# Kernel optimization log

Measured on AMD Instinct MI355X. Metric: run time of the kernel, lower is better.

## Reference

```python
import jax, jax.numpy as jnp
import numpy as np

B_, L_, D_MODEL, D_STATE, D_CONV, EXPAND, N_BLOCKS = 2, 2048, 512, 16, 4, 2, 4
D_INNER = EXPAND * D_MODEL            # 1024
DT_RANK = (D_MODEL + 15) // 16        # 32 (ceil(d_model/16))


def setup_inputs() -> dict:
    key = jax.random.key(0)
    ks = jax.random.split(key, 8)
    s = 0.02
    n = N_BLOCKS
    x = jax.random.normal(ks[0], (B_, L_, D_MODEL), jnp.float32)
    W_in = jax.random.normal(ks[1], (n, D_MODEL, 2 * D_INNER), jnp.float32) * s
    conv_w = jax.random.normal(ks[2], (n, D_INNER, D_CONV), jnp.float32) * s
    conv_b = jnp.zeros((n, D_INNER), jnp.float32)
    W_x = jax.random.normal(ks[3], (n, D_INNER, DT_RANK + 2 * D_STATE), jnp.float32) * s
    W_dt = jax.random.normal(ks[4], (n, DT_RANK, D_INNER), jnp.float32) * s
    # dt bias so softplus(b_dt) gives small positive timesteps (standard Mamba init range)
    b_dt = jax.random.uniform(ks[5], (n, D_INNER), jnp.float32, minval=-4.6, maxval=-2.3)
    # A_log init: log(1..d_state) per channel (S4D-real init)
    A_log = jnp.log(jnp.broadcast_to(jnp.arange(1, D_STATE + 1, dtype=jnp.float32), (n, D_INNER, D_STATE)))
    Dp = jnp.ones((n, D_INNER), jnp.float32)
    W_out = jax.random.normal(ks[6], (n, D_INNER, D_MODEL), jnp.float32) * s
    return {"x": x, "W_in": W_in, "conv_w": conv_w, "conv_b": conv_b,
            "W_x": W_x, "W_dt": W_dt, "b_dt": b_dt, "A_log": A_log,
            "Dp": Dp, "W_out": W_out}


def _scan_combine(e1, e2):
    a1, b1 = e1
    a2, b2 = e2
    return a1 * a2, a2 * b1 + b2


def _mamba_block(x, W_in, conv_w, conv_b, W_x, W_dt, b_dt, A_log, Dp, W_out):
    # x: [B, L, d_model]
    xz = x @ W_in                                   # [B, L, 2*d_inner]
    xi, z = jnp.split(xz, 2, axis=-1)
    # causal depthwise conv over time (torch pads d_conv-1 then truncates to L)
    xc = jnp.transpose(xi, (0, 2, 1))               # [B, d_inner, L]
    w = conv_w[:, None, :]                          # [d_inner, 1, d_conv]
    xc = jax.lax.conv_general_dilated(
        xc, w, window_strides=(1,), padding=[(D_CONV - 1, 0)],
        dimension_numbers=("NCH", "OIH", "NCH"), feature_group_count=D_INNER)
    xc = xc + conv_b[None, :, None]
    xc = jax.nn.silu(jnp.transpose(xc, (0, 2, 1)))  # [B, L, d_inner]
    # input-dependent dt, B, C
    dbc = xc @ W_x                                  # [B, L, dt_rank + 2*d_state]
    dt_raw = dbc[..., :DT_RANK]
    Bs = dbc[..., DT_RANK:DT_RANK + D_STATE]        # [B, L, d_state]
    Cs = dbc[..., DT_RANK + D_STATE:]               # [B, L, d_state]
    dt = jax.nn.softplus(dt_raw @ W_dt + b_dt)      # [B, L, d_inner]
    A = -jnp.exp(A_log)                             # [d_inner, d_state]
    # discretized selective scan terms
    dA = jnp.exp(dt[..., None] * A)                 # [B, L, d_inner, d_state]
    dBx = (dt * xc)[..., None] * Bs[:, :, None, :]  # [B, L, d_inner, d_state]
    # parallel associative scan over time: h_t = dA_t * h_{t-1} + dBx_t
    _, h = jax.lax.associative_scan(_scan_combine, (dA, dBx), axis=1)
    y = jnp.einsum("blds,bls->bld", h, Cs) + xc * Dp
    y = y * jax.nn.silu(z)
    return y @ W_out                                # [B, L, d_model]


def reference(x, W_in, conv_w, conv_b, W_x, W_dt, b_dt, A_log, Dp, W_out):
    for i in range(N_BLOCKS):
        resid = x
        x = _mamba_block(x, W_in[i], conv_w[i], conv_b[i], W_x[i], W_dt[i],
                         b_dt[i], A_log[i], Dp[i], W_out[i])
        x = x + resid
    return x
```

## Files before the change

### kernel.cpp

```cpp
#include <hip/hip_runtime.h>


#define L_    2048
#define DM    512
#define DI    1024
#define DS    16
#define NBLK  4
#define NC    64
#define CH    32
#define MROWS 4096

using u16 = unsigned short;
typedef __bf16 bf16x8 __attribute__((ext_vector_type(8)));
typedef float  f32x4  __attribute__((ext_vector_type(4)));

__device__ __forceinline__ float b2f(u16 u) {
    union { unsigned int i; float f; } v; v.i = ((unsigned int)u) << 16; return v.f;
}
__device__ __forceinline__ u16 f2b(float f) {
    union { float f; unsigned int i; } v; v.f = f;
    unsigned int x = v.i;
    return (u16)((x + 0x7FFFu + ((x >> 16) & 1u)) >> 16);
}
__device__ __forceinline__ float silu_(float x) { return x / (1.f + __expf(-x)); }

struct F4 { float x, y, z, w; };
__device__ __forceinline__ F4 load4(const void* p, size_t e, bool isbf) {
    F4 r;
    if (isbf) {
        ushort4 v = *(const ushort4*)((const u16*)p + e);
        r.x = b2f(v.x); r.y = b2f(v.y); r.z = b2f(v.z); r.w = b2f(v.w);
    } else {
        float4 v = *(const float4*)((const float*)p + e);
        r.x = v.x; r.y = v.y; r.z = v.z; r.w = v.w;
    }
    return r;
}
__device__ __forceinline__ float load1(const void* p, size_t e, bool isbf) {
    return isbf ? b2f(((const u16*)p)[e]) : ((const float*)p)[e];
}

__device__ __forceinline__ void async16(const u16* g, u16* l) {
    __builtin_amdgcn_global_load_lds(
        (const __attribute__((address_space(1))) unsigned int*)g,
        (__attribute__((address_space(3))) unsigned int*)l, 16, 0, 0);
}

__global__ void probe_dtype(const void* x, float* flag) {
    __shared__ int allok;
    if (threadIdx.x == 0) allok = 1;
    __syncthreads();
    const u16* p = (const u16*)x;
    bool ok = true;
    for (int i = threadIdx.x; i < 2048; i += 256) {
        float v = b2f(p[i]);
        if (!(v == v) || fabsf(v) >= 1000.f) ok = false;
    }
    if (!ok) allok = 0;
    __syncthreads();
    if (threadIdx.x == 0) flag[0] = allok ? 1.f : 0.f;
}

__global__ __launch_bounds__(256) void transpose_wb(
    const void* __restrict__ src, int R, int C,
    u16* __restrict__ dst, const float* __restrict__ flagp)
{
    const bool isbf = (*flagp > 0.5f);
    __shared__ u16 t[32][33];
    const size_t mo = (size_t)blockIdx.z * R * C;
    const int c0 = blockIdx.x * 32, r0 = blockIdx.y * 32;
    const int tx = threadIdx.x & 31, ty = threadIdx.x >> 5;
    #pragma unroll
    for (int i = 0; i < 32; i += 8)
        t[ty + i][tx] = f2b(load1(src, mo + (size_t)(r0 + ty + i) * C + c0 + tx, isbf));
    __syncthreads();
    #pragma unroll
    for (int i = 0; i < 32; i += 8)
        dst[mo + (size_t)(c0 + ty + i) * R + r0 + tx] = t[tx][ty + i];
}

template<int BN, int MT, int OM>
__global__ __launch_bounds__(256) void gemm_lds(
    const u16* __restrict__ A, int lda,
    const u16* __restrict__ BT, int Kd,
    u16* __restrict__ Cb, float* __restrict__ Cf, int ldc,
    const float* __restrict__ resid)
{
    constexpr int BM = 32 * MT;
    constexpr int NT = BN / 32;
    constexpr int W  = NT * 16;
    constexpr int CA = BM * 4;
    constexpr int T  = CA + BN * 4;
    constexpr int PW = T / 4;
    constexpr int NI = PW / 64;
    constexpr int STG = (BM + BN) * 32;
    constexpr int EPI = 4 * 16 * (W + 4) * 2;
    constexpr int LN  = STG > EPI ? STG : EPI;
    __shared__ u16 sL[LN];
    u16* sA = sL;
    u16* sB = sL + BM * 32;
    const int tid = threadIdx.x;
    const int lane = tid & 63;
    const int wid = tid >> 6;
    const int wm = wid >> 1, wn = wid & 1;
    const int m0 = blockIdx.y * BM;
    const int n0 = blockIdx.x * BN;
    const int col16 = lane & 15, quad = lane >> 4;

    f32x4 acc[MT][NT];
    #pragma unroll
    for (int i = 0; i < MT; i++)
        #pragma unroll
        for (int j = 0; j < NT; j++) acc[i][j] = {0.f, 0.f, 0.f, 0.f};

    for (int k0 = 0; k0 < Kd; k0 += 32) {
        #pragma unroll
        for (int it = 0; it < NI; it++) {
            const int cbase = wid * PW + it * 64;
            const int c = cbase + lane;
            const u16* g;
            if (cbase < CA)
                g = A + (size_t)(m0 + (c >> 2)) * lda + k0 + ((c & 3) << 3);
            else {
                const int cc = c - CA;
                g = BT + (size_t)(n0 + (cc >> 2)) * Kd + k0 + ((cc & 3) << 3);
            }
            async16(g, sL + (size_t)cbase * 8);
        }
        __syncthreads();
        bf16x8 af[MT], bfr[NT];
        #pragma unroll
        for (int mi = 0; mi < MT; mi++)
            af[mi] = *(const bf16x8*)&sA[(wm * 16 * MT + mi * 16 + col16) * 32 + quad * 8];
        #pragma unroll
        for (int ni = 0; ni < NT; ni++)
            bfr[ni] = *(const bf16x8*)&sB[(wn * (BN / 2) + ni * 16 + col16) * 32 + quad * 8];
        #pragma unroll
        for (int mi = 0; mi < MT; mi++)
            #pragma unroll
            for (int ni = 0; ni < NT; ni++)
                acc[mi][ni] = __builtin_amdgcn_mfma_f32_16x16x32_bf16(
                    af[mi], bfr[ni], acc[mi][ni], 0, 0, 0);
        __syncthreads();
    }

    __syncthreads();
    float* sw = (float*)sL + wid * 16 * (W + 4);
    constexpr int LPR = W / 8;
    constexpr int RPP = 64 / LPR;
    constexpr int NP  = 16 / RPP;
    #pragma unroll
    for (int mi = 0; mi < MT; mi++) {
        #pragma unroll
        for (int ni = 0; ni < NT; ni++)
            #pragma unroll
            for (int rr = 0; rr < 4; rr++)
                sw[(quad * 4 + rr) * (W + 4) + ni * 16 + col16] = acc[mi][ni][rr];
        #pragma unroll
        for (int p = 0; p < NP; p++) {
            const int row = p * RPP + lane / LPR;
            const int colg = (lane % LPR) * 8;
            float4 v0 = *(const float4*)&sw[row * (W + 4) + colg];
            float4 v1 = *(const float4*)&sw[row * (W + 4) + colg + 4];
            const int grow = m0 + wm * 16 * MT + mi * 16 + row;
            const int gcol = n0 + wn * (BN / 2) + colg;
            if (OM == 2) {
                const float4 r0 = *(const float4*)&resid[(size_t)grow * ldc + gcol];
                const float4 r1 = *(const float4*)&resid[(size_t)grow * ldc + gcol + 4];
                v0.x += r0.x; v0.y += r0.y; v0.z += r0.z; v0.w += r0.w;
                v1.x += r1.x; v1.y += r1.y; v1.z += r1.z; v1.w += r1.w;
                *(float4*)&Cf[(size_t)grow * ldc + gcol]     = v0;
                *(float4*)&Cf[(size_t)grow * ldc + gcol + 4] = v1;
            }
            ushort4 b0 = make_ushort4(f2b(v0.x), f2b(v0.y), f2b(v0.z), f2b(v0.w));
            ushort4 b1 = make_ushort4(f2b(v1.x), f2b(v1.y), f2b(v1.z), f2b(v1.w));
            *(ushort4*)&Cb[(size_t)grow * ldc + gcol]     = b0;
            *(ushort4*)&Cb[(size_t)grow * ldc + gcol + 4] = b1;
        }
    }
}

template<int BN, int MT>
__global__ __launch_bounds__(256) void gemm_bf(
    const u16* __restrict__ A, int lda,
    const u16* __restrict__ BT, int Kd,
    float* __restrict__ Cf, int ldc)
{
    constexpr int NT = BN / 32;
    constexpr int BM = 32 * MT;
    constexpr int ASL = BM * 4;
    constexpr int AIT = (ASL + 255) / 256;
    constexpr int BSL = BN * 4;
    constexpr int BIT = (BSL + 255) / 256;
    __shared__ u16 sA[BM][40];
    __shared__ u16 sB[BN][40];
    const int tid = threadIdx.x;
    const int lane = tid & 63;
    const int wid = tid >> 6;
    const int wm = wid >> 1, wn = wid & 1;
    const int m0 = blockIdx.y * BM;
    const int n0 = blockIdx.x * BN;
    const int col16 = lane & 15, quad = lane >> 4;

    f32x4 acc[MT][NT];
    #pragma unroll
    for (int i = 0; i < MT; i++)
        #pragma unroll
        for (int j = 0; j < NT; j++) acc[i][j] = {0.f, 0.f, 0.f, 0.f};

    int4 fa[AIT], fb[BIT];
    #pragma unroll
    for (int it = 0; it < AIT; it++) {
        const int slot = tid + it * 256;
        if (slot < ASL)
            fa[it] = *(const int4*)&A[(size_t)(m0 + (slot >> 2)) * lda + ((slot & 3) << 3)];
    }
    #pragma unroll
    for (int it = 0; it < BIT; it++) {
        const int slot = tid + it * 256;
        if (slot < BSL)
            fb[it] = *(const int4*)&BT[(size_t)(n0 + (slot >> 2)) * Kd + ((slot & 3) << 3)];
    }

    for (int k0 = 0;;) {
        __syncthreads();
        #pragma unroll
        for (int it = 0; it < AIT; it++) {
            const int slot = tid + it * 256;
            if (slot < ASL) *(int4*)&sA[slot >> 2][(slot & 3) << 3] = fa[it];
        }
        #pragma unroll
        for (int it = 0; it < BIT; it++) {
            const int slot = tid + it * 256;
            if (slot < BSL) *(int4*)&sB[slot >> 2][(slot & 3) << 3] = fb[it];
        }
        __syncthreads();
        k0 += 32;
        const bool more = (k0 < Kd);
        if (more) {
            #pragma unroll
            for (int it = 0; it < AIT; it++) {
                const int slot = tid + it * 256;
                if (slot < ASL)
                    fa[it] = *(const int4*)&A[(size_t)(m0 + (slot >> 2)) * lda + k0 + ((slot & 3) << 3)];
            }
            #pragma unroll
            for (int it = 0; it < BIT; it++) {
                const int slot = tid + it * 256;
                if (slot < BSL)
                    fb[it] = *(const int4*)&BT[(size_t)(n0 + (slot >> 2)) * Kd + k0 + ((slot & 3) << 3)];
            }
        }
        bf16x8 af[MT], bfr[NT];
        #pragma unroll
        for (int mi = 0; mi < MT; mi++)
            af[mi] = *(const bf16x8*)&sA[wm * (16 * MT) + mi * 16 + col16][quad * 8];
        #pragma unroll
        for (int ni = 0; ni < NT; ni++)
            bfr[ni] = *(const bf16x8*)&sB[wn * (BN / 2) + ni * 16 + col16][quad * 8];
        #pragma unroll
        for (int mi = 0; mi < MT; mi++)
            #pragma unroll
            for (int ni = 0; ni < NT; ni++)
                acc[mi][ni] = __builtin_amdgcn_mfma_f32_16x16x32_bf16(
                    af[mi], bfr[ni], acc[mi][ni], 0, 0, 0);
        if (!more) break;
    }
    #pragma unroll
    for (int mi = 0; mi < MT; mi++)
        #pragma unroll
        for (int ni = 0; ni < NT; ni++)
            #pragma unroll
            for (int rr = 0; rr < 4; rr++) {
                const int row = m0 + wm * (16 * MT) + mi * 16 + quad * 4 + rr;
                const int col = n0 + wn * (BN / 2) + ni * 16 + col16;
                Cf[(size_t)row * ldc + col] = acc[mi][ni][rr];
            }
}

__global__ __launch_bounds__(256) void conv_silu(
    const u16* __restrict__ xz, const void* __restrict__ cw, size_t cwo,
    const void* __restrict__ cb, size_t cbo, u16* __restrict__ xc,
    const float* __restrict__ flagp)
{
    const bool isbf = (*flagp > 0.5f);
    const int idx = blockIdx.x * 256 + threadIdx.x;
    const int d = idx & (DI - 1);
    const int row = idx >> 10;
    const int l = row & (L_ - 1);
    const F4 wv = load4(cw, cwo + (size_t)d * 4, isbf);
    const u16* base = xz + (size_t)row * 2048 + d;
    float acc = load1(cb, cbo + d, isbf) + wv.w * b2f(base[0]);
    if (l >= 1) acc += wv.z * b2f(base[-2048]);
    if (l >= 2) acc += wv.y * b2f(base[-4096]);
    if (l >= 3) acc += wv.x * b2f(base[-6144]);
    xc[idx] = f2b(silu_(acc));
}

__global__ __launch_bounds__(256) void scan_phase1(
    const u16* __restrict__ xcb, const float* __restrict__ dbc,
    const void* __restrict__ Wdt, size_t wdto,
    const void* __restrict__ bdt, size_t bdto,
    const void* __restrict__ Alog, size_t alo,
    float* __restrict__ Sdt, float* __restrict__ Sbuf,
    const float* __restrict__ flagp)
{
    const bool isbf = (*flagp > 0.5f);
    __shared__ float sD[CH][64];
    const int blk = blockIdx.x;
    const int dblk = blk & 3;
    const int c = (blk >> 2) & (NC - 1);
    const int b = blk >> 8;
    const int d = dblk * 256 + threadIdx.x;
    const int row0 = b * L_ + c * CH;
    #pragma unroll
    for (int t = threadIdx.x; t < CH * 16; t += 256) {
        const int r = t >> 4, c4 = (t & 15) << 2;
        *(float4*)&sD[r][c4] = *(const float4*)&dbc[(size_t)(row0 + r) * 64 + c4];
    }
    __syncthreads();
    float wdt[32];
    #pragma unroll
    for (int r = 0; r < 32; r++) wdt[r] = load1(Wdt, wdto + (size_t)r * DI + d, isbf);
    const float bdtv = load1(bdt, bdto + d, isbf);
    float A[DS], h[DS];
    #pragma unroll
    for (int s = 0; s < DS; s++) { A[s] = -__expf(load1(Alog, alo + (size_t)d * DS + s, isbf)); h[s] = 0.f; }
    float sdt = 0.f;
    for (int l = 0; l < CH; l++) {
        float dtr = bdtv;
        #pragma unroll
        for (int r = 0; r < 32; r++) dtr = fmaf(sD[l][r], wdt[r], dtr);
        const float dt = (dtr > 20.f) ? dtr : __logf(1.f + __expf(dtr));
        const float xv = b2f(xcb[(size_t)(row0 + l) * DI + d]);
        sdt += dt;
        const float dtx = dt * xv;
        #pragma unroll
        for (int s = 0; s < DS; s++)
            h[s] = fmaf(__expf(dt * A[s]), h[s], dtx * sD[l][32 + s]);
    }
    const int cb_ = b * NC + c;
    Sdt[(size_t)cb_ * DI + d] = sdt;
    #pragma unroll
    for (int s = 0; s < DS; s++) Sbuf[((size_t)cb_ * DS + s) * DI + d] = h[s];
}

__global__ __launch_bounds__(256) void scan_phase2(
    const float* __restrict__ Sdt, float* __restrict__ Sbuf,
    const void* __restrict__ Alog, size_t alo,
    const float* __restrict__ flagp)
{
    const bool isbf = (*flagp > 0.5f);
    const int g = blockIdx.x * 256 + threadIdx.x;
    const int d = g & (DI - 1);
    const int s = (g >> 10) & (DS - 1);
    const int b = g >> 14;
    const float A = -__expf(load1(Alog, alo + (size_t)d * DS + s, isbf));
    float h = 0.f;
    for (int c = 0; c < NC; c++) {
        const int cb_ = b * NC + c;
        const size_t idx = ((size_t)cb_ * DS + s) * DI + d;
        const float tmp = Sbuf[idx];
        Sbuf[idx] = h;
        const float P = __expf(A * Sdt[(size_t)cb_ * DI + d]);
        h = fmaf(P, h, tmp);
    }
}

__global__ __launch_bounds__(256) void scan_phase3(
    u16* __restrict__ xcb, const float* __restrict__ dbc,
    const void* __restrict__ Wdt, size_t wdto,
    const void* __restrict__ bdt, size_t bdto,
    const void* __restrict__ Alog, size_t alo,
    const float* __restrict__ H0, const void* __restrict__ Dpv, size_t dpo,
    const u16* __restrict__ xz, const float* __restrict__ flagp)
{
    const bool isbf = (*flagp > 0.5f);
    __shared__ float sD[CH][64];
    const int blk = blockIdx.x;
    const int dblk = blk & 3;
    const int c = (blk >> 2) & (NC - 1);
    const int b = blk >> 8;
    const int d = dblk * 256 + threadIdx.x;
    const int row0 = b * L_ + c * CH;
    #pragma unroll
    for (int t = threadIdx.x; t < CH * 16; t += 256) {
        const int r = t >> 4, c4 = (t & 15) << 2;
        *(float4*)&sD[r][c4] = *(const float4*)&dbc[(size_t)(row0 + r) * 64 + c4];
    }
    __syncthreads();
    float wdt[32];
    #pragma unroll
    for (int r = 0; r < 32; r++) wdt[r] = load1(Wdt, wdto + (size_t)r * DI + d, isbf);
    const float bdtv = load1(bdt, bdto + d, isbf);
    float A[DS], h[DS];
    const int cb_ = b * NC + c;
    #pragma unroll
    for (int s = 0; s < DS; s++) {
        A[s] = -__expf(load1(Alog, alo + (size_t)d * DS + s, isbf));
        h[s] = H0[((size_t)cb_ * DS + s) * DI + d];
    }
    const float Dpd = load1(Dpv, dpo + d, isbf);
    for (int l = 0; l < CH; l++) {
        float dtr = bdtv;
        #pragma unroll
        for (int r = 0; r < 32; r++) dtr = fmaf(sD[l][r], wdt[r], dtr);
        const float dt = (dtr > 20.f) ? dtr : __logf(1.f + __expf(dtr));
        const int row = row0 + l;
        const float xv = b2f(xcb[(size_t)row * DI + d]);
        const float dtx = dt * xv;
        float y = 0.f;
        #pragma unroll
        for (int s = 0; s < DS; s++) {
            h[s] = fmaf(__expf(dt * A[s]), h[s], dtx * sD[l][32 + s]);
            y = fmaf(h[s], sD[l][48 + s], y);
        }
        y = fmaf(xv, Dpd, y);
        y *= silu_(b2f(xz[(size_t)row * 2048 + DI + d]));
        xcb[(size_t)row * DI + d] = f2b(y);
    }
}

__global__ void cast_in(const void* __restrict__ in, float* __restrict__ outf,
                        u16* __restrict__ outb, int n, const float* __restrict__ flagp) {
    const bool isbf = (*flagp > 0.5f);
    const int i = blockIdx.x * 256 + threadIdx.x;
    if (i < n) {
        const float v = load1(in, (size_t)i, isbf);
        outf[i] = v;
        outb[i] = f2b(v);
    }
}
__global__ void cast_out(const float* __restrict__ in, void* __restrict__ out, int n,
                         const float* __restrict__ flagp) {
    const bool isbf = (*flagp > 0.5f);
    const int i = blockIdx.x * 256 + threadIdx.x;
    if (i < n) {
        if (isbf) ((u16*)out)[i] = f2b(in[i]);
        else      ((float*)out)[i] = in[i];
    }
}

extern "C" void kernel_launch(void* const* d_in, const int* in_sizes, int n_in,
                              void* d_out, int out_size, void* d_ws, size_t ws_size,
                              hipStream_t stream)
{
    const void* x_in  = d_in[0];
    const void* W_in  = d_in[1];
    const void* convw = d_in[2];
    const void* convb = d_in[3];
    const void* W_x   = d_in[4];
    const void* W_dt  = d_in[5];
    const void* b_dt  = d_in[6];
    const void* A_log = d_in[7];
    const void* Dp    = d_in[8];
    const void* W_out = d_in[9];

    char* base = (char*)d_ws;
    float* flag  = (float*)base;                     base += 16;
    u16*   xz    = (u16*)base;                       base += (size_t)MROWS * 2048 * 2;
    u16*   xc    = (u16*)base;                       base += (size_t)MROWS * DI * 2;
    u16*   xb_bf = (u16*)base;                       base += (size_t)MROWS * DM * 2;
    float* dbc   = (float*)base;                     base += (size_t)MROWS * 64 * 4;
    float* Sdt   = (float*)base;                     base += (size_t)2 * NC * DI * 4;
    float* Sbuf  = (float*)base;                     base += (size_t)2 * NC * DS * DI * 4;
    float* xb_f  = (float*)base;                     base += (size_t)MROWS * DM * 4;
    u16*   WinT  = (u16*)base;                       base += (size_t)NBLK * 2048 * DM * 2;
    u16*   WxT   = (u16*)base;                       base += (size_t)NBLK * 64 * DI * 2;
    u16*   WoutT = (u16*)base;                       base += (size_t)NBLK * DM * DI * 2;

    probe_dtype<<<1, 256, 0, stream>>>(x_in, flag);
    transpose_wb<<<dim3(2048 / 32, DM / 32, NBLK), 256, 0, stream>>>(W_in, DM, 2048, WinT, flag);
    transpose_wb<<<dim3(64 / 32, DI / 32, NBLK), 256, 0, stream>>>(W_x, DI, 64, WxT, flag);
    transpose_wb<<<dim3(DM / 32, DI / 32, NBLK), 256, 0, stream>>>(W_out, DI, DM, WoutT, flag);
    cast_in<<<(MROWS * DM) / 256, 256, 0, stream>>>(x_in, xb_f, xb_bf, MROWS * DM, flag);

    for (int i = 0; i < NBLK; i++) {
        gemm_lds<128, 4, 0><<<dim3(2048 / 128, MROWS / 128), 256, 0, stream>>>(
            xb_bf, DM, WinT + (size_t)i * 2048 * DM, DM, xz, nullptr, 2048, nullptr);
        conv_silu<<<(MROWS * DI) / 256, 256, 0, stream>>>(
            xz, convw, (size_t)i * DI * 4, convb, (size_t)i * DI, xc, flag);
        gemm_bf<64, 1><<<dim3(1, MROWS / 32), 256, 0, stream>>>(
            xc, DI, WxT + (size_t)i * 64 * DI, DI, dbc, 64);
        scan_phase1<<<2 * NC * 4, 256, 0, stream>>>(
            xc, dbc, W_dt, (size_t)i * 32 * DI, b_dt, (size_t)i * DI,
            A_log, (size_t)i * DI * DS, Sdt, Sbuf, flag);
        scan_phase2<<<128, 256, 0, stream>>>(Sdt, Sbuf, A_log, (size_t)i * DI * DS, flag);
        scan_phase3<<<2 * NC * 4, 256, 0, stream>>>(
            xc, dbc, W_dt, (size_t)i * 32 * DI, b_dt, (size_t)i * DI,
            A_log, (size_t)i * DI * DS, Sbuf, Dp, (size_t)i * DI, xz, flag);
        gemm_lds<64, 2, 2><<<dim3(DM / 64, MROWS / 64), 256, 0, stream>>>(
            xc, DI, WoutT + (size_t)i * DM * DI, DI, xb_bf, xb_f, DM, xb_f);
    }
    cast_out<<<(MROWS * DM) / 256, 256, 0, stream>>>(xb_f, d_out, MROWS * DM, flag);
}
```

Baseline: 667.1 us.

## Fuse scan phases into cooperative kernel, vectorize conv, fold output cast into GEMM

The three scan phases are merged into one cooperative kernel that uses grid-wide syncs. Phase 3 now reads dt from shared memory instead of recomputing it, and two kernel launches are dropped per block. The depthwise conv handles four channels per thread with vector loads. The W_x GEMM is split across two column blocks. The last block's output GEMM writes straight to the output in the probed dtype, which removes the separate cast kernel. In exchange, the cooperative launch needs all 512 blocks to be resident at once, and the extra shared memory could limit occupancy.

```diff
diff --git a/kernel.cpp b/kernel.cpp
--- a/kernel.cpp
+++ b/kernel.cpp
@@ -1,4 +1,5 @@
 #include <hip/hip_runtime.h>
+#include <hip/hip_cooperative_groups.h>
 
 
 #define L_    2048
@@ -10,6 +11,7 @@
 #define CH    32
 #define MROWS 4096
 
+namespace cg = cooperative_groups;
 using u16 = unsigned short;
 typedef __bf16 bf16x8 __attribute__((ext_vector_type(8)));
 typedef float  f32x4  __attribute__((ext_vector_type(4)));
@@ -84,7 +86,8 @@
     const u16* __restrict__ A, int lda,
     const u16* __restrict__ BT, int Kd,
     u16* __restrict__ Cb, float* __restrict__ Cf, int ldc,
-    const float* __restrict__ resid)
+    const float* __restrict__ resid,
+    const float* __restrict__ flagp)
 {
     constexpr int BM = 32 * MT;
     constexpr int NT = BN / 32;
@@ -106,6 +109,7 @@
     const int m0 = blockIdx.y * BM;
     const int n0 = blockIdx.x * BN;
     const int col16 = lane & 15, quad = lane >> 4;
+    const bool isbf = (OM == 3) ? (*flagp > 0.5f) : false;
 
     f32x4 acc[MT][NT];
     #pragma unroll
@@ -164,18 +168,25 @@
             float4 v1 = *(const float4*)&sw[row * (W + 4) + colg + 4];
             const int grow = m0 + wm * 16 * MT + mi * 16 + row;
             const int gcol = n0 + wn * (BN / 2) + colg;
-            if (OM == 2) {
+            if (OM == 2 || OM == 3) {
                 const float4 r0 = *(const float4*)&resid[(size_t)grow * ldc + gcol];
                 const float4 r1 = *(const float4*)&resid[(size_t)grow * ldc + gcol + 4];
                 v0.x += r0.x; v0.y += r0.y; v0.z += r0.z; v0.w += r0.w;
                 v1.x += r1.x; v1.y += r1.y; v1.z += r1.z; v1.w += r1.w;
+            }
+            if (OM == 2) {
                 *(float4*)&Cf[(size_t)grow * ldc + gcol]     = v0;
                 *(float4*)&Cf[(size_t)grow * ldc + gcol + 4] = v1;
             }
-            ushort4 b0 = make_ushort4(f2b(v0.x), f2b(v0.y), f2b(v0.z), f2b(v0.w));
-            ushort4 b1 = make_ushort4(f2b(v1.x), f2b(v1.y), f2b(v1.z), f2b(v1.w));
-            *(ushort4*)&Cb[(size_t)grow * ldc + gcol]     = b0;
-            *(ushort4*)&Cb[(size_t)grow * ldc + gcol + 4] = b1;
+            if (OM == 3 && !isbf) {
+                *(float4*)&Cf[(size_t)grow * ldc + gcol]     = v0;
+                *(float4*)&Cf[(size_t)grow * ldc + gcol + 4] = v1;
+            } else {
+                ushort4 b0 = make_ushort4(f2b(v0.x), f2b(v0.y), f2b(v0.z), f2b(v0.w));
+                ushort4 b1 = make_ushort4(f2b(v1.x), f2b(v1.y), f2b(v1.z), f2b(v1.w));
+                *(ushort4*)&Cb[(size_t)grow * ldc + gcol]     = b0;
+                *(ushort4*)&Cb[(size_t)grow * ldc + gcol + 4] = b1;
+            }
         }
     }
 }
@@ -284,37 +295,52 @@
     const float* __restrict__ flagp)
 {
     const bool isbf = (*flagp > 0.5f);
-    const int idx = blockIdx.x * 256 + threadIdx.x;
-    const int d = idx & (DI - 1);
-    const int row = idx >> 10;
+    const int t = blockIdx.x * 256 + threadIdx.x;
+    const int d = (t & 255) << 2;
+    const int row = t >> 8;
     const int l = row & (L_ - 1);
-    const F4 wv = load4(cw, cwo + (size_t)d * 4, isbf);
+    const F4 w0 = load4(cw, cwo + (size_t)d * 4, isbf);
+    const F4 w1 = load4(cw, cwo + (size_t)d * 4 + 4, isbf);
+    const F4 w2 = load4(cw, cwo + (size_t)d * 4 + 8, isbf);
+    const F4 w3 = load4(cw, cwo + (size_t)d * 4 + 12, isbf);
+    const F4 bias = load4(cb, cbo + d, isbf);
     const u16* base = xz + (size_t)row * 2048 + d;
-    float acc = load1(cb, cbo + d, isbf) + wv.w * b2f(base[0]);
-    if (l >= 1) acc += wv.z * b2f(base[-2048]);
-    if (l >= 2) acc += wv.y * b2f(base[-4096]);
-    if (l >= 3) acc += wv.x * b2f(base[-6144]);
-    xc[idx] = f2b(silu_(acc));
-}
-
-__global__ __launch_bounds__(256) void scan_phase1(
-    const u16* __restrict__ xcb, const float* __restrict__ dbc,
-    const void* __restrict__ Wdt, size_t wdto,
-    const void* __restrict__ bdt, size_t bdto,
-    const void* __restrict__ Alog, size_t alo,
+    const ushort4 x0 = *(const ushort4*)&base[0];
+    float a0 = bias.x + w0.w * b2f(x0.x);
+    float a1 = bias.y + w1.w * b2f(x0.y);
+    float a2 = bias.z + w2.w * b2f(x0.z);
+    float a3 = bias.w + w3.w * b2f(x0.w);
+    if (l >= 1) { const ushort4 v = *(const ushort4*)&base[-2048];
+        a0 += w0.z * b2f(v.x); a1 += w1.z * b2f(v.y); a2 += w2.z * b2f(v.z); a3 += w3.z * b2f(v.w); }
+    if (l >= 2) { const ushort4 v = *(const ushort4*)&base[-4096];
+        a0 += w0.y * b2f(v.x); a1 += w1.y * b2f(v.y); a2 += w2.y * b2f(v.z); a3 += w3.y * b2f(v.w); }
+    if (l >= 3) { const ushort4 v = *(const ushort4*)&base[-6144];
+        a0 += w0.x * b2f(v.x); a1 += w1.x * b2f(v.y); a2 += w2.x * b2f(v.z); a3 += w3.x * b2f(v.w); }
+    ushort4 o = make_ushort4(f2b(silu_(a0)), f2b(silu_(a1)), f2b(silu_(a2)), f2b(silu_(a3)));
+    *(ushort4*)&xc[(size_t)row * DI + d] = o;
+}
+
+__global__ __launch_bounds__(256) void scan_fused(
+    u16* __restrict__ xcb, const float* __restrict__ dbc,
+    const void* __restrict__ Wdt, unsigned long wdto,
+    const void* __restrict__ bdt, unsigned long bdto,
+    const void* __restrict__ Alog, unsigned long alo,
     float* __restrict__ Sdt, float* __restrict__ Sbuf,
-    const float* __restrict__ flagp)
-{
+    const void* __restrict__ Dpv, unsigned long dpo,
+    const u16* __restrict__ xz, const float* __restrict__ flagp)
+{
+    cg::grid_group grid = cg::this_grid();
     const bool isbf = (*flagp > 0.5f);
     __shared__ float sD[CH][64];
+    __shared__ float sDt[CH * 256];
+    const int tid = threadIdx.x;
     const int blk = blockIdx.x;
     const int dblk = blk & 3;
     const int c = (blk >> 2) & (NC - 1);
     const int b = blk >> 8;
-    const int d = dblk * 256 + threadIdx.x;
+    const int d = dblk * 256 + tid;
     const int row0 = b * L_ + c * CH;
-    #pragma unroll
-    for (int t = threadIdx.x; t < CH * 16; t += 256) {
+    for (int t = tid; t < CH * 16; t += 256) {
         const int r = t >> 4, c4 = (t & 15) << 2;
         *(float4*)&sD[r][c4] = *(const float4*)&dbc[(size_t)(row0 + r) * 64 + c4];
     }
@@ -325,13 +351,17 @@
     const float bdtv = load1(bdt, bdto + d, isbf);
     float A[DS], h[DS];
     #pragma unroll
-    for (int s = 0; s < DS; s++) { A[s] = -__expf(load1(Alog, alo + (size_t)d * DS + s, isbf)); h[s] = 0.f; }
+    for (int s = 0; s < DS; s++) {
+        A[s] = -__expf(load1(Alog, alo + (size_t)d * DS + s, isbf));
+        h[s] = 0.f;
+    }
     float sdt = 0.f;
     for (int l = 0; l < CH; l++) {
         float dtr = bdtv;
         #pragma unroll
         for (int r = 0; r < 32; r++) dtr = fmaf(sD[l][r], wdt[r], dtr);
         const float dt = (dtr > 20.f) ? dtr : __logf(1.f + __expf(dtr));
+        sDt[l * 256 + tid] = dt;
         const float xv = b2f(xcb[(size_t)(row0 + l) * DI + d]);
         sdt += dt;
         const float dtx = dt * xv;
@@ -343,69 +373,33 @@
     Sdt[(size_t)cb_ * DI + d] = sdt;
     #pragma unroll
     for (int s = 0; s < DS; s++) Sbuf[((size_t)cb_ * DS + s) * DI + d] = h[s];
-}
-
-__global__ __launch_bounds__(256) void scan_phase2(
-    const float* __restrict__ Sdt, float* __restrict__ Sbuf,
-    const void* __restrict__ Alog, size_t alo,
-    const float* __restrict__ flagp)
-{
-    const bool isbf = (*flagp > 0.5f);
-    const int g = blockIdx.x * 256 + threadIdx.x;
-    const int d = g & (DI - 1);
-    const int s = (g >> 10) & (DS - 1);
-    const int b = g >> 14;
-    const float A = -__expf(load1(Alog, alo + (size_t)d * DS + s, isbf));
-    float h = 0.f;
-    for (int c = 0; c < NC; c++) {
-        const int cb_ = b * NC + c;
-        const size_t idx = ((size_t)cb_ * DS + s) * DI + d;
-        const float tmp = Sbuf[idx];
-        Sbuf[idx] = h;
-        const float P = __expf(A * Sdt[(size_t)cb_ * DI + d]);
-        h = fmaf(P, h, tmp);
-    }
-}
-
-__global__ __launch_bounds__(256) void scan_phase3(
-    u16* __restrict__ xcb, const float* __restrict__ dbc,
-    const void* __restrict__ Wdt, size_t wdto,
-    const void* __restrict__ bdt, size_t bdto,
-    const void* __restrict__ Alog, size_t alo,
-    const float* __restrict__ H0, const void* __restrict__ Dpv, size_t dpo,
-    const u16* __restrict__ xz, const float* __restrict__ flagp)
-{
-    const bool isbf = (*flagp > 0.5f);
-    __shared__ float sD[CH][64];
-    const int blk = blockIdx.x;
-    const int dblk = blk & 3;
-    const int c = (blk >> 2) & (NC - 1);
-    const int b = blk >> 8;
-    const int d = dblk * 256 + threadIdx.x;
-    const int row0 = b * L_ + c * CH;
-    #pragma unroll
-    for (int t = threadIdx.x; t < CH * 16; t += 256) {
-        const int r = t >> 4, c4 = (t & 15) << 2;
-        *(float4*)&sD[r][c4] = *(const float4*)&dbc[(size_t)(row0 + r) * 64 + c4];
-    }
-    __syncthreads();
-    float wdt[32];
-    #pragma unroll
-    for (int r = 0; r < 32; r++) wdt[r] = load1(Wdt, wdto + (size_t)r * DI + d, isbf);
-    const float bdtv = load1(bdt, bdto + d, isbf);
-    float A[DS], h[DS];
-    const int cb_ = b * NC + c;
-    #pragma unroll
-    for (int s = 0; s < DS; s++) {
-        A[s] = -__expf(load1(Alog, alo + (size_t)d * DS + s, isbf));
-        h[s] = H0[((size_t)cb_ * DS + s) * DI + d];
-    }
+
+    grid.sync();
+
+    const int g = blk * 256 + tid;
+    if (g < 2 * DS * DI) {
+        const int d2 = g & (DI - 1);
+        const int s2 = (g >> 10) & (DS - 1);
+        const int b2 = g >> 14;
+        const float A2 = -__expf(load1(Alog, alo + (size_t)d2 * DS + s2, isbf));
+        float hh = 0.f;
+        for (int c2 = 0; c2 < NC; c2++) {
+            const int cb2 = b2 * NC + c2;
+            const size_t idx = ((size_t)cb2 * DS + s2) * DI + d2;
+            const float tmp = Sbuf[idx];
+            Sbuf[idx] = hh;
+            const float P = __expf(A2 * Sdt[(size_t)cb2 * DI + d2]);
+            hh = fmaf(P, hh, tmp);
+        }
+    }
+
+    grid.sync();
+
+    #pragma unroll
+    for (int s = 0; s < DS; s++) h[s] = Sbuf[((size_t)cb_ * DS + s) * DI + d];
     const float Dpd = load1(Dpv, dpo + d, isbf);
     for (int l = 0; l < CH; l++) {
-        float dtr = bdtv;
-        #pragma unroll
-        for (int r = 0; r < 32; r++) dtr = fmaf(sD[l][r], wdt[r], dtr);
-        const float dt = (dtr > 20.f) ? dtr : __logf(1.f + __expf(dtr));
+        const float dt = sDt[l * 256 + tid];
         const int row = row0 + l;
         const float xv = b2f(xcb[(size_t)row * DI + d]);
         const float dtx = dt * xv;
@@ -429,15 +423,6 @@
         const float v = load1(in, (size_t)i, isbf);
         outf[i] = v;
         outb[i] = f2b(v);
-    }
-}
-__global__ void cast_out(const float* __restrict__ in, void* __restrict__ out, int n,
-                         const float* __restrict__ flagp) {
-    const bool isbf = (*flagp > 0.5f);
-    const int i = blockIdx.x * 256 + threadIdx.x;
-    if (i < n) {
-        if (isbf) ((u16*)out)[i] = f2b(in[i]);
-        else      ((float*)out)[i] = in[i];
     }
 }
 
@@ -477,20 +462,28 @@
 
     for (int i = 0; i < NBLK; i++) {
         gemm_lds<128, 4, 0><<<dim3(2048 / 128, MROWS / 128), 256, 0, stream>>>(
-            xb_bf, DM, WinT + (size_t)i * 2048 * DM, DM, xz, nullptr, 2048, nullptr);
-        conv_silu<<<(MROWS * DI) / 256, 256, 0, stream>>>(
+            xb_bf, DM, WinT + (size_t)i * 2048 * DM, DM, xz, nullptr, 2048, nullptr, flag);
+        conv_silu<<<(MROWS * DI / 4) / 256, 256, 0, stream>>>(
             xz, convw, (size_t)i * DI * 4, convb, (size_t)i * DI, xc, flag);
-        gemm_bf<64, 1><<<dim3(1, MROWS / 32), 256, 0, stream>>>(
+        gemm_bf<32, 1><<<dim3(2, MROWS / 32), 256, 0, stream>>>(
             xc, DI, WxT + (size_t)i * 64 * DI, DI, dbc, 64);
-        scan_phase1<<<2 * NC * 4, 256, 0, stream>>>(
-            xc, dbc, W_dt, (size_t)i * 32 * DI, b_dt, (size_t)i * DI,
-            A_log, (size_t)i * DI * DS, Sdt, Sbuf, flag);
-        scan_phase2<<<128, 256, 0, stream>>>(Sdt, Sbuf, A_log, (size_t)i * DI * DS, flag);
-        scan_phase3<<<2 * NC * 4, 256, 0, stream>>>(
-            xc, dbc, W_dt, (size_t)i * 32 * DI, b_dt, (size_t)i * DI,
-            A_log, (size_t)i * DI * DS, Sbuf, Dp, (size_t)i * DI, xz, flag);
-        gemm_lds<64, 2, 2><<<dim3(DM / 64, MROWS / 64), 256, 0, stream>>>(
-            xc, DI, WoutT + (size_t)i * DM * DI, DI, xb_bf, xb_f, DM, xb_f);
-    }
-    cast_out<<<(MROWS * DM) / 256, 256, 0, stream>>>(xb_f, d_out, MROWS * DM, flag);
-}
+        {
+            unsigned long wdto = (size_t)i * 32 * DI, bdto = (size_t)i * DI;
+            unsigned long alo = (size_t)i * DI * DS, dpo = (size_t)i * DI;
+            void* sargs[] = {(void*)&xc, (void*)&dbc, (void*)&W_dt, (void*)&wdto,
+                             (void*)&b_dt, (void*)&bdto, (void*)&A_log, (void*)&alo,
+                             (void*)&Sdt, (void*)&Sbuf, (void*)&Dp, (void*)&dpo,
+                             (void*)&xz, (void*)&flag};
+            hipLaunchCooperativeKernel((const void*)scan_fused, dim3(2 * NC * 4), dim3(256),
+                                       sargs, 0, stream);
+        }
+        if (i == NBLK - 1) {
+            gemm_lds<64, 2, 3><<<dim3(DM / 64, MROWS / 64), 256, 0, stream>>>(
+                xc, DI, WoutT + (size_t)i * DM * DI, DI, (u16*)d_out, (float*)d_out, DM,
+                xb_f, flag);
+        } else {
+            gemm_lds<64, 2, 2><<<dim3(DM / 64, MROWS / 64), 256, 0, stream>>>(
+                xc, DI, WoutT + (size_t)i * DM * DI, DI, xb_bf, xb_f, DM, xb_f, flag);
+        }
+    }
+}
```

After: 1.143 ms. 1.71x slower.

## Fuse output cast into last GEMM, vectorize conv, split x-proj GEMM columns

Applied to the files above, without the earlier changes.

The final out-projection GEMM now adds the residual and writes straight to the output buffer in the input dtype, which removes the separate cast_out kernel. The conv+SiLU kernel handles four channels per thread with ushort4 loads and stores. The x-projection GEMM uses BN=32 tiles with twice the blocks to raise parallelism. The new epilogue mode reads a dtype flag per block.

```diff
diff --git a/kernel.cpp b/kernel.cpp
--- a/kernel.cpp
+++ b/kernel.cpp
@@ -84,7 +84,8 @@
     const u16* __restrict__ A, int lda,
     const u16* __restrict__ BT, int Kd,
     u16* __restrict__ Cb, float* __restrict__ Cf, int ldc,
-    const float* __restrict__ resid)
+    const float* __restrict__ resid,
+    const float* __restrict__ flagp)
 {
     constexpr int BM = 32 * MT;
     constexpr int NT = BN / 32;
@@ -106,6 +107,7 @@
     const int m0 = blockIdx.y * BM;
     const int n0 = blockIdx.x * BN;
     const int col16 = lane & 15, quad = lane >> 4;
+    const bool isbf = (OM == 3) ? (*flagp > 0.5f) : false;
 
     f32x4 acc[MT][NT];
     #pragma unroll
@@ -164,18 +166,25 @@
             float4 v1 = *(const float4*)&sw[row * (W + 4) + colg + 4];
             const int grow = m0 + wm * 16 * MT + mi * 16 + row;
             const int gcol = n0 + wn * (BN / 2) + colg;
-            if (OM == 2) {
+            if (OM == 2 || OM == 3) {
                 const float4 r0 = *(const float4*)&resid[(size_t)grow * ldc + gcol];
                 const float4 r1 = *(const float4*)&resid[(size_t)grow * ldc + gcol + 4];
                 v0.x += r0.x; v0.y += r0.y; v0.z += r0.z; v0.w += r0.w;
                 v1.x += r1.x; v1.y += r1.y; v1.z += r1.z; v1.w += r1.w;
+            }
+            if (OM == 2) {
                 *(float4*)&Cf[(size_t)grow * ldc + gcol]     = v0;
                 *(float4*)&Cf[(size_t)grow * ldc + gcol + 4] = v1;
             }
-            ushort4 b0 = make_ushort4(f2b(v0.x), f2b(v0.y), f2b(v0.z), f2b(v0.w));
-            ushort4 b1 = make_ushort4(f2b(v1.x), f2b(v1.y), f2b(v1.z), f2b(v1.w));
-            *(ushort4*)&Cb[(size_t)grow * ldc + gcol]     = b0;
-            *(ushort4*)&Cb[(size_t)grow * ldc + gcol + 4] = b1;
+            if (OM == 3 && !isbf) {
+                *(float4*)&Cf[(size_t)grow * ldc + gcol]     = v0;
+                *(float4*)&Cf[(size_t)grow * ldc + gcol + 4] = v1;
+            } else {
+                ushort4 b0 = make_ushort4(f2b(v0.x), f2b(v0.y), f2b(v0.z), f2b(v0.w));
+                ushort4 b1 = make_ushort4(f2b(v1.x), f2b(v1.y), f2b(v1.z), f2b(v1.w));
+                *(ushort4*)&Cb[(size_t)grow * ldc + gcol]     = b0;
+                *(ushort4*)&Cb[(size_t)grow * ldc + gcol + 4] = b1;
+            }
         }
     }
 }
@@ -284,17 +293,29 @@
     const float* __restrict__ flagp)
 {
     const bool isbf = (*flagp > 0.5f);
-    const int idx = blockIdx.x * 256 + threadIdx.x;
-    const int d = idx & (DI - 1);
-    const int row = idx >> 10;
+    const int t = blockIdx.x * 256 + threadIdx.x;
+    const int d = (t & 255) << 2;
+    const int row = t >> 8;
     const int l = row & (L_ - 1);
-    const F4 wv = load4(cw, cwo + (size_t)d * 4, isbf);
+    const F4 w0 = load4(cw, cwo + (size_t)d * 4, isbf);
+    const F4 w1 = load4(cw, cwo + (size_t)d * 4 + 4, isbf);
+    const F4 w2 = load4(cw, cwo + (size_t)d * 4 + 8, isbf);
+    const F4 w3 = load4(cw, cwo + (size_t)d * 4 + 12, isbf);
+    const F4 bias = load4(cb, cbo + d, isbf);
     const u16* base = xz + (size_t)row * 2048 + d;
-    float acc = load1(cb, cbo + d, isbf) + wv.w * b2f(base[0]);
-    if (l >= 1) acc += wv.z * b2f(base[-2048]);
-    if (l >= 2) acc += wv.y * b2f(base[-4096]);
-    if (l >= 3) acc += wv.x * b2f(base[-6144]);
-    xc[idx] = f2b(silu_(acc));
+    const ushort4 x0 = *(const ushort4*)&base[0];
+    float a0 = bias.x + w0.w * b2f(x0.x);
+    float a1 = bias.y + w1.w * b2f(x0.y);
+    float a2 = bias.z + w2.w * b2f(x0.z);
+    float a3 = bias.w + w3.w * b2f(x0.w);
+    if (l >= 1) { const ushort4 v = *(const ushort4*)&base[-2048];
+        a0 += w0.z * b2f(v.x); a1 += w1.z * b2f(v.y); a2 += w2.z * b2f(v.z); a3 += w3.z * b2f(v.w); }
+    if (l >= 2) { const ushort4 v = *(const ushort4*)&base[-4096];
+        a0 += w0.y * b2f(v.x); a1 += w1.y * b2f(v.y); a2 += w2.y * b2f(v.z); a3 += w3.y * b2f(v.w); }
+    if (l >= 3) { const ushort4 v = *(const ushort4*)&base[-6144];
+        a0 += w0.x * b2f(v.x); a1 += w1.x * b2f(v.y); a2 += w2.x * b2f(v.z); a3 += w3.x * b2f(v.w); }
+    ushort4 o = make_ushort4(f2b(silu_(a0)), f2b(silu_(a1)), f2b(silu_(a2)), f2b(silu_(a3)));
+    *(ushort4*)&xc[(size_t)row * DI + d] = o;
 }
 
 __global__ __launch_bounds__(256) void scan_phase1(
@@ -431,15 +452,6 @@
         outb[i] = f2b(v);
     }
 }
-__global__ void cast_out(const float* __restrict__ in, void* __restrict__ out, int n,
-                         const float* __restrict__ flagp) {
-    const bool isbf = (*flagp > 0.5f);
-    const int i = blockIdx.x * 256 + threadIdx.x;
-    if (i < n) {
-        if (isbf) ((u16*)out)[i] = f2b(in[i]);
-        else      ((float*)out)[i] = in[i];
-    }
-}
 
 extern "C" void kernel_launch(void* const* d_in, const int* in_sizes, int n_in,
                               void* d_out, int out_size, void* d_ws, size_t ws_size,
@@ -477,10 +489,10 @@
 
     for (int i = 0; i < NBLK; i++) {
         gemm_lds<128, 4, 0><<<dim3(2048 / 128, MROWS / 128), 256, 0, stream>>>(
-            xb_bf, DM, WinT + (size_t)i * 2048 * DM, DM, xz, nullptr, 2048, nullptr);
-        conv_silu<<<(MROWS * DI) / 256, 256, 0, stream>>>(
+            xb_bf, DM, WinT + (size_t)i * 2048 * DM, DM, xz, nullptr, 2048, nullptr, flag);
+        conv_silu<<<(MROWS * DI / 4) / 256, 256, 0, stream>>>(
             xz, convw, (size_t)i * DI * 4, convb, (size_t)i * DI, xc, flag);
-        gemm_bf<64, 1><<<dim3(1, MROWS / 32), 256, 0, stream>>>(
+        gemm_bf<32, 1><<<dim3(2, MROWS / 32), 256, 0, stream>>>(
             xc, DI, WxT + (size_t)i * 64 * DI, DI, dbc, 64);
         scan_phase1<<<2 * NC * 4, 256, 0, stream>>>(
             xc, dbc, W_dt, (size_t)i * 32 * DI, b_dt, (size_t)i * DI,
@@ -489,8 +501,13 @@
         scan_phase3<<<2 * NC * 4, 256, 0, stream>>>(
             xc, dbc, W_dt, (size_t)i * 32 * DI, b_dt, (size_t)i * DI,
             A_log, (size_t)i * DI * DS, Sbuf, Dp, (size_t)i * DI, xz, flag);
-        gemm_lds<64, 2, 2><<<dim3(DM / 64, MROWS / 64), 256, 0, stream>>>(
-            xc, DI, WoutT + (size_t)i * DM * DI, DI, xb_bf, xb_f, DM, xb_f);
-    }
-    cast_out<<<(MROWS * DM) / 256, 256, 0, stream>>>(xb_f, d_out, MROWS * DM, flag);
-}
+        if (i == NBLK - 1) {
+            gemm_lds<64, 2, 3><<<dim3(DM / 64, MROWS / 64), 256, 0, stream>>>(
+                xc, DI, WoutT + (size_t)i * DM * DI, DI, (u16*)d_out, (float*)d_out, DM,
+                xb_f, flag);
+        } else {
+            gemm_lds<64, 2, 2><<<dim3(DM / 64, MROWS / 64), 256, 0, stream>>>(
+                xc, DI, WoutT + (size_t)i * DM * DI, DI, xb_bf, xb_f, DM, xb_f, flag);
+        }
+    }
+}
```

Result: faster. 652.8 us (-2.1%).
